# Performance work log

Measured on AMD Instinct MI355X. Metric: run time of the kernel, lower is better.

## Reference

```python
import jax, jax.numpy as jnp
import numpy as np

D = 1024
K = 64
H = 8           # MHA heads
HD = D // H
TEMP = 0.1
B, S = 8, 4096


def setup_inputs() -> dict:
    key = jax.random.key(0)
    ks = jax.random.split(key, 16)
    s = lambda fan_in: 1.0 / np.sqrt(fan_in)
    inp = {
        "x": jax.random.normal(ks[0], (B, S, D), dtype=jnp.float32),
        "efas_scores": jax.random.uniform(ks[1], (B, S), dtype=jnp.float32),
        # energy_projector: Linear(1 -> K)
        "w_e": jax.random.uniform(ks[2], (K,), minval=-1.0, maxval=1.0, dtype=jnp.float32),
        "b_e": jax.random.uniform(ks[3], (K,), minval=-1.0, maxval=1.0, dtype=jnp.float32),
        # routing_mlp: Linear(D->K), ReLU, Linear(K->K); weights stored [in, out]
        "w1": jax.random.uniform(ks[4], (D, K), minval=-s(D), maxval=s(D), dtype=jnp.float32),
        "b1": jax.random.uniform(ks[5], (K,), minval=-s(D), maxval=s(D), dtype=jnp.float32),
        "w2": jax.random.uniform(ks[6], (K, K), minval=-s(K), maxval=s(K), dtype=jnp.float32),
        "b2": jax.random.uniform(ks[7], (K,), minval=-s(K), maxval=s(K), dtype=jnp.float32),
        # MultiheadAttention packed in-proj [D, 3D] and out-proj [D, D]
        "w_qkv": jax.random.uniform(ks[8], (D, 3 * D), minval=-s(D), maxval=s(D), dtype=jnp.float32),
        "b_qkv": jnp.zeros((3 * D,), dtype=jnp.float32),
        "w_o": jax.random.uniform(ks[9], (D, D), minval=-s(D), maxval=s(D), dtype=jnp.float32),
        "b_o": jnp.zeros((D,), dtype=jnp.float32),
        # output_proj: Linear(D -> D)
        "w_p": jax.random.uniform(ks[10], (D, D), minval=-s(D), maxval=s(D), dtype=jnp.float32),
        "b_p": jax.random.uniform(ks[11], (D,), minval=-s(D), maxval=s(D), dtype=jnp.float32),
    }
    return inp


def _mha(a, w_qkv, b_qkv, w_o, b_o):
    # a: [B, K, D] self-attention, 8 heads (eval mode, no dropout)
    b, k, _ = a.shape
    qkv = a @ w_qkv + b_qkv                         # [B, K, 3D]
    q, kk, v = jnp.split(qkv, 3, axis=-1)
    split = lambda t: t.reshape(b, k, H, HD).transpose(0, 2, 1, 3)  # [B,H,K,HD]
    q, kk, v = split(q), split(kk), split(v)
    scores = jnp.einsum('bhqd,bhkd->bhqk', q, kk) / np.sqrt(HD)
    attn = jax.nn.softmax(scores, axis=-1)
    out = jnp.einsum('bhqk,bhkd->bhqd', attn, v)    # [B,H,K,HD]
    out = out.transpose(0, 2, 1, 3).reshape(b, k, D)
    return out @ w_o + b_o


def reference(x, efas_scores, w_e, b_e, w1, b1, w2, b2, w_qkv, b_qkv, w_o, b_o, w_p, b_p):
    # energy routing: Linear(1 -> K) on efas_scores[..., None]
    energy_routing = efas_scores[..., None] * w_e + b_e            # [B,S,K]
    # content routing: Linear(D->K) -> ReLU -> Linear(K->K)
    content_routing = jax.nn.relu(x @ w1 + b1) @ w2 + b2           # [B,S,K]
    # eval-mode combination as in the original (self.training == False)
    routing_logits = energy_routing * 2.0 + content_routing
    routing_weights = jax.nn.softmax(routing_logits / TEMP, axis=-1)  # [B,S,K]
    # token -> anchor weighted aggregation
    anchor_inputs = jnp.einsum('bsk,bsd->bkd', routing_weights, x)    # [B,K,D]
    anchor_outputs = _mha(anchor_inputs, w_qkv, b_qkv, w_o, b_o)      # [B,K,D]
    # anchor -> token scatter-back
    token_outputs = jnp.einsum('bsk,bkd->bsd', routing_weights, anchor_outputs)
    return token_outputs @ w_p + b_p
```

## Files before the change

### kernel.cpp

```cpp
#include <hip/hip_runtime.h>
#include <cstddef>

#define TB 256

constexpr int Bb = 8, Ss = 4096, Dd = 1024, Kk = 64, Hh = 8;
constexpr float INV_TEMP = 10.0f;
constexpr float ATTN_SCALE = 0.08838834764831845f;

constexpr size_t N_RW  = (size_t)Bb * Ss * Kk;
constexpr size_t N_AKD = (size_t)Bb * Kk * Dd;
constexpr size_t OFF_RW  = 0;
constexpr size_t OFF_AI  = OFF_RW  + N_RW;
constexpr size_t OFF_QKV = OFF_AI  + N_AKD;
constexpr size_t OFF_ATT = OFF_QKV + 3 * N_AKD;
constexpr size_t OFF_AO  = OFF_ATT + N_AKD;
constexpr size_t OFF_AOP = OFF_AO  + N_AKD;

typedef __attribute__((ext_vector_type(8))) short bf16x8;
typedef __attribute__((ext_vector_type(4))) float f32x4;

#define MFMA(a, b, c) __builtin_amdgcn_mfma_f32_16x16x32_bf16(a, b, c, 0, 0, 0)

__device__ inline ushort f2bf(float f) {
    union { float f; uint u; } v; v.f = f;
    return (ushort)((v.u + 0x7fffu + ((v.u >> 16) & 1u)) >> 16);
}
__device__ inline float bf2f(ushort h) {
    union { uint u; float f; } v; v.u = ((uint)h) << 16;
    return v.f;
}
__device__ inline void split2(float f, ushort& h, ushort& l) {
    h = f2bf(f);
    l = f2bf(f - bf2f(h));
}

__device__ inline void st4(ushort* t, int row, int s0, ushort4 v) {
    char* p = (char*)t + row * 144 + ((((s0 >> 3) ^ ((row >> 2) & 7)) << 4) | ((s0 & 7) << 1));
    *(ushort4*)p = v;
}
__device__ inline void st1(ushort* t, int row, int s, ushort v) {
    char* p = (char*)t + row * 144 + ((((s >> 3) ^ ((row >> 2) & 7)) << 4) | ((s & 7) << 1));
    *(ushort*)p = v;
}
__device__ inline bf16x8 ldfrag(const ushort* t, int row, int sblk) {
    const char* p = (const char*)t + row * 144 + (((sblk ^ ((row >> 2) & 7))) << 4);
    return *(const bf16x8*)p;
}
__device__ inline void natf(ushort* thi, ushort* tlo, int row, int s0, float4 v) {
    ushort h0,h1,h2,h3,l0,l1,l2,l3;
    split2(v.x,h0,l0); split2(v.y,h1,l1); split2(v.z,h2,l2); split2(v.w,h3,l3);
    st4(thi, row, s0, make_ushort4(h0,h1,h2,h3));
    st4(tlo, row, s0, make_ushort4(l0,l1,l2,l3));
}
__device__ inline void trf(ushort* thi, ushort* tlo, int rowbase, int s0,
                           float4 a, float4 b, float4 c, float4 d) {
    float m[4][4] = {{a.x,b.x,c.x,d.x},{a.y,b.y,c.y,d.y},
                     {a.z,b.z,c.z,d.z},{a.w,b.w,c.w,d.w}};
#pragma unroll
    for (int i = 0; i < 4; ++i) {
        ushort h[4], l[4];
#pragma unroll
        for (int j = 0; j < 4; ++j) split2(m[i][j], h[j], l[j]);
        st4(thi, rowbase + i, s0, make_ushort4(h[0],h[1],h[2],h[3]));
        st4(tlo, rowbase + i, s0, make_ushort4(l[0],l[1],l[2],l[3]));
    }
}
__device__ inline f32x4 mm3(bf16x8 ah, bf16x8 al, bf16x8 bh, bf16x8 bl, f32x4 c) {
    c = MFMA(ah, bh, c);
    c = MFMA(ah, bl, c);
    c = MFMA(al, bh, c);
    return c;
}

__global__ __launch_bounds__(TB) void k_zero(float* __restrict__ p, int n4) {
    int i = blockIdx.x * TB + threadIdx.x;
    if (i < n4) ((float4*)p)[i] = make_float4(0.f, 0.f, 0.f, 0.f);
}

__global__ __launch_bounds__(TB) void k_routing(
    const float* __restrict__ x, const float* __restrict__ efas,
    const float* __restrict__ w_e, const float* __restrict__ b_e,
    const float* __restrict__ w1, const float* __restrict__ b1,
    const float* __restrict__ w2, const float* __restrict__ b2,
    float* __restrict__ rw)
{
    __shared__ __align__(16) ushort xa_hi[128*72], xa_lo[128*72];
    __shared__ __align__(16) ushort wa_hi[64*72],  wa_lo[64*72];
    const int tid = threadIdx.x, lane = tid & 63, wv = tid >> 6;
    const int b = blockIdx.x & 7, t0 = (blockIdx.x >> 3) * 128;
    const int r15 = lane & 15, g = lane >> 4;

    f32x4 acc[2][4];
#pragma unroll
    for (int mt = 0; mt < 2; ++mt)
#pragma unroll
      for (int nt = 0; nt < 4; ++nt) acc[mt][nt] = (f32x4)0.f;

    for (int kc = 0; kc < 16; ++kc) {
        const int k0 = kc * 64;
#pragma unroll
        for (int p = 0; p < 8; ++p) {
            int q = tid + p * TB;
            int row = q >> 4, s0 = (q & 15) << 2;
            float4 v = *(const float4*)&x[((size_t)b*Ss + t0 + row)*Dd + k0 + s0];
            natf(xa_hi, xa_lo, row, s0, v);
        }
        {
            int n0 = (tid & 15) << 2, s0 = (tid >> 4) << 2;
            const float* base = &w1[(size_t)(k0 + s0) * Kk + n0];
            float4 a  = *(const float4*)(base);
            float4 bq = *(const float4*)(base + Kk);
            float4 cq = *(const float4*)(base + 2*Kk);
            float4 dq = *(const float4*)(base + 3*Kk);
            trf(wa_hi, wa_lo, n0, s0, a, bq, cq, dq);
        }
        __syncthreads();
#pragma unroll
        for (int ks = 0; ks < 2; ++ks) {
            bf16x8 ah[2], al[2];
#pragma unroll
            for (int mt = 0; mt < 2; ++mt) {
                int row = wv*32 + mt*16 + r15;
                ah[mt] = ldfrag(xa_hi, row, ks*4 + g);
                al[mt] = ldfrag(xa_lo, row, ks*4 + g);
            }
#pragma unroll
            for (int nt = 0; nt < 4; ++nt) {
                bf16x8 bh = ldfrag(wa_hi, nt*16 + r15, ks*4 + g);
                bf16x8 bl = ldfrag(wa_lo, nt*16 + r15, ks*4 + g);
#pragma unroll
                for (int mt = 0; mt < 2; ++mt)
                    acc[mt][nt] = mm3(ah[mt], al[mt], bh, bl, acc[mt][nt]);
            }
        }
        __syncthreads();
    }
    float b1v[4];
#pragma unroll
    for (int nt = 0; nt < 4; ++nt) b1v[nt] = b1[nt*16 + r15];
#pragma unroll
    for (int mt = 0; mt < 2; ++mt)
#pragma unroll
      for (int nt = 0; nt < 4; ++nt)
#pragma unroll
        for (int j = 0; j < 4; ++j) {
            float hv = fmaxf(acc[mt][nt][j] + b1v[nt], 0.f);
            ushort hh, hl; split2(hv, hh, hl);
            int row = wv*32 + mt*16 + g*4 + j, col = nt*16 + r15;
            st1(xa_hi, row, col, hh);
            st1(xa_lo, row, col, hl);
        }
    {
        int n0 = (tid & 15) << 2, s0 = (tid >> 4) << 2;
        const float* base = &w2[(size_t)s0 * Kk + n0];
        float4 a  = *(const float4*)(base);
        float4 bq = *(const float4*)(base + Kk);
        float4 cq = *(const float4*)(base + 2*Kk);
        float4 dq = *(const float4*)(base + 3*Kk);
        trf(wa_hi, wa_lo, n0, s0, a, bq, cq, dq);
    }
    __syncthreads();

    f32x4 acc2[2][4];
#pragma unroll
    for (int mt = 0; mt < 2; ++mt)
#pragma unroll
      for (int nt = 0; nt < 4; ++nt) acc2[mt][nt] = (f32x4)0.f;
#pragma unroll
    for (int ks = 0; ks < 2; ++ks) {
        bf16x8 ah[2], al[2];
#pragma unroll
        for (int mt = 0; mt < 2; ++mt) {
            int row = wv*32 + mt*16 + r15;
            ah[mt] = ldfrag(xa_hi, row, ks*4 + g);
            al[mt] = ldfrag(xa_lo, row, ks*4 + g);
        }
#pragma unroll
        for (int nt = 0; nt < 4; ++nt) {
            bf16x8 bh = ldfrag(wa_hi, nt*16 + r15, ks*4 + g);
            bf16x8 bl = ldfrag(wa_lo, nt*16 + r15, ks*4 + g);
#pragma unroll
            for (int mt = 0; mt < 2; ++mt)
                acc2[mt][nt] = mm3(ah[mt], al[mt], bh, bl, acc2[mt][nt]);
        }
    }
    float wev[4], bev[4], b2v[4];
#pragma unroll
    for (int nt = 0; nt < 4; ++nt) {
        wev[nt] = w_e[nt*16 + r15]; bev[nt] = b_e[nt*16 + r15]; b2v[nt] = b2[nt*16 + r15];
    }
#pragma unroll
    for (int mt = 0; mt < 2; ++mt)
#pragma unroll
      for (int j = 0; j < 4; ++j) {
        int row = wv*32 + mt*16 + g*4 + j;
        float ef = efas[(size_t)b*Ss + t0 + row];
        float t[4];
#pragma unroll
        for (int nt = 0; nt < 4; ++nt)
            t[nt] = (acc2[mt][nt][j] + b2v[nt] + 2.f*(ef*wev[nt] + bev[nt])) * INV_TEMP;
        float m = fmaxf(fmaxf(t[0],t[1]), fmaxf(t[2],t[3]));
#pragma unroll
        for (int off = 1; off <= 8; off <<= 1) m = fmaxf(m, __shfl_xor(m, off));
        float s = 0.f;
#pragma unroll
        for (int nt = 0; nt < 4; ++nt) { t[nt] = __expf(t[nt] - m); s += t[nt]; }
#pragma unroll
        for (int off = 1; off <= 8; off <<= 1) s += __shfl_xor(s, off);
        float inv = 1.f / s;
#pragma unroll
        for (int nt = 0; nt < 4; ++nt)
            rw[((size_t)b*Ss + t0 + row)*Kk + nt*16 + r15] = t[nt] * inv;
      }
}

__global__ __launch_bounds__(TB) void k_anchor(
    const float* __restrict__ x, const float* __restrict__ rw, float* __restrict__ ai)
{
    __shared__ __align__(16) ushort at_hi[64*72],  at_lo[64*72];
    __shared__ __align__(16) ushort bt_hi[128*72], bt_lo[128*72];
    const int tid = threadIdx.x, lane = tid & 63, wv = tid >> 6;
    const int b = blockIdx.x & 7, dt = (blockIdx.x >> 3) & 7, sc = blockIdx.x >> 6;
    const int r15 = lane & 15, g = lane >> 4;

    f32x4 acc[4][2];
#pragma unroll
    for (int mt = 0; mt < 4; ++mt)
#pragma unroll
      for (int nt = 0; nt < 2; ++nt) acc[mt][nt] = (f32x4)0.f;

    for (int cc = 0; cc < 8; ++cc) {
        const int sb = sc*512 + cc*64;
        {
            int k0 = (tid & 15) << 2, s0 = (tid >> 4) << 2;
            const float* base = &rw[((size_t)b*Ss + sb + s0)*Kk + k0];
            float4 a  = *(const float4*)(base);
            float4 bq = *(const float4*)(base + Kk);
            float4 cq = *(const float4*)(base + 2*Kk);
            float4 dq = *(const float4*)(base + 3*Kk);
            trf(at_hi, at_lo, k0, s0, a, bq, cq, dq);
        }
#pragma unroll
        for (int p = 0; p < 2; ++p) {
            int q = tid + p * TB;
            int d0 = (q & 31) << 2, s0 = (q >> 5) << 2;
            const float* base = &x[((size_t)b*Ss + sb + s0)*Dd + dt*128 + d0];
            float4 a  = *(const float4*)(base);
            float4 bq = *(const float4*)(base + Dd);
            float4 cq = *(const float4*)(base + 2*Dd);
            float4 dq = *(const float4*)(base + 3*Dd);
            trf(bt_hi, bt_lo, d0, s0, a, bq, cq, dq);
        }
        __syncthreads();
#pragma unroll
        for (int ks = 0; ks < 2; ++ks) {
            bf16x8 ah[4], al[4];
#pragma unroll
            for (int mt = 0; mt < 4; ++mt) {
                ah[mt] = ldfrag(at_hi, mt*16 + r15, ks*4 + g);
                al[mt] = ldfrag(at_lo, mt*16 + r15, ks*4 + g);
            }
#pragma unroll
            for (int nt = 0; nt < 2; ++nt) {
                int rn = wv*32 + nt*16 + r15;
                bf16x8 bh = ldfrag(bt_hi, rn, ks*4 + g);
                bf16x8 bl = ldfrag(bt_lo, rn, ks*4 + g);
#pragma unroll
                for (int mt = 0; mt < 4; ++mt)
                    acc[mt][nt] = mm3(ah[mt], al[mt], bh, bl, acc[mt][nt]);
            }
        }
        __syncthreads();
    }
#pragma unroll
    for (int mt = 0; mt < 4; ++mt)
#pragma unroll
      for (int nt = 0; nt < 2; ++nt)
#pragma unroll
        for (int j = 0; j < 4; ++j) {
            int k = mt*16 + g*4 + j;
            int d = dt*128 + wv*32 + nt*16 + r15;
            atomicAdd(&ai[((size_t)b*Kk + k)*Dd + d], acc[mt][nt][j]);
        }
}

template <int KDIM, int NDIM, bool HASBIAS>
__global__ __launch_bounds__(TB) void k_gemm_a(
    const float* __restrict__ A, const float* __restrict__ W,
    const float* __restrict__ bias, float* __restrict__ C)
{
    __shared__ __align__(16) ushort at_hi[64*72],  at_lo[64*72];
    __shared__ __align__(16) ushort bt_hi[128*72], bt_lo[128*72];
    const int tid = threadIdx.x, lane = tid & 63, wv = tid >> 6;
    const int b = blockIdx.x & 7, n0 = (blockIdx.x >> 3) * 128;
    const int r15 = lane & 15, g = lane >> 4;

    f32x4 acc[4][2];
#pragma unroll
    for (int mt = 0; mt < 4; ++mt)
#pragma unroll
      for (int nt = 0; nt < 2; ++nt) acc[mt][nt] = (f32x4)0.f;

    for (int kc = 0; kc < KDIM/64; ++kc) {
        const int k0 = kc * 64;
#pragma unroll
        for (int p = 0; p < 4; ++p) {
            int q = tid + p * TB;
            int row = q >> 4, s0 = (q & 15) << 2;
            float4 v = *(const float4*)&A[((size_t)b*64 + row)*KDIM + k0 + s0];
            natf(at_hi, at_lo, row, s0, v);
        }
#pragma unroll
        for (int p = 0; p < 2; ++p) {
            int q = tid + p * TB;
            int nn0 = (q & 31) << 2, s0 = (q >> 5) << 2;
            const float* base = &W[(size_t)(k0 + s0)*NDIM + n0 + nn0];
            float4 a  = *(const float4*)(base);
            float4 bq = *(const float4*)(base + NDIM);
            float4 cq = *(const float4*)(base + 2*(size_t)NDIM);
            float4 dq = *(const float4*)(base + 3*(size_t)NDIM);
            trf(bt_hi, bt_lo, nn0, s0, a, bq, cq, dq);
        }
        __syncthreads();
#pragma unroll
        for (int ks = 0; ks < 2; ++ks) {
            bf16x8 ah[4], al[4];
#pragma unroll
            for (int mt = 0; mt < 4; ++mt) {
                ah[mt] = ldfrag(at_hi, mt*16 + r15, ks*4 + g);
                al[mt] = ldfrag(at_lo, mt*16 + r15, ks*4 + g);
            }
#pragma unroll
            for (int nt = 0; nt < 2; ++nt) {
                int rn = wv*32 + nt*16 + r15;
                bf16x8 bh = ldfrag(bt_hi, rn, ks*4 + g);
                bf16x8 bl = ldfrag(bt_lo, rn, ks*4 + g);
#pragma unroll
                for (int mt = 0; mt < 4; ++mt)
                    acc[mt][nt] = mm3(ah[mt], al[mt], bh, bl, acc[mt][nt]);
            }
        }
        __syncthreads();
    }
#pragma unroll
    for (int nt = 0; nt < 2; ++nt) {
        int n = n0 + wv*32 + nt*16 + r15;
        float bb = HASBIAS ? bias[n] : 0.f;
#pragma unroll
        for (int mt = 0; mt < 4; ++mt)
#pragma unroll
          for (int j = 0; j < 4; ++j)
            C[((size_t)b*64 + mt*16 + g*4 + j)*NDIM + n] = acc[mt][nt][j] + bb;
    }
}

__global__ __launch_bounds__(TB) void k_attn(
    const float* __restrict__ qkv, float* __restrict__ att)
{
    __shared__ __align__(16) ushort qt_hi[64*72],  qt_lo[64*72];
    __shared__ __align__(16) ushort kt_hi[64*72],  kt_lo[64*72];
    __shared__ __align__(16) ushort vt_hi[128*72], vt_lo[128*72];
    const int tid = threadIdx.x, lane = tid & 63, wv = tid >> 6;
    const int b = blockIdx.x >> 3, h = blockIdx.x & 7;
    const int r15 = lane & 15, g = lane >> 4;

    f32x4 accs[4];
#pragma unroll
    for (int nt = 0; nt < 4; ++nt) accs[nt] = (f32x4)0.f;

    for (int ch = 0; ch < 2; ++ch) {
        const int c0 = h*128 + ch*64;
#pragma unroll
        for (int p = 0; p < 4; ++p) {
            int q = tid + p * TB;
            int row = q >> 4, s0 = (q & 15) << 2;
            size_t base = ((size_t)b*64 + row)*3072 + c0 + s0;
            natf(qt_hi, qt_lo, row, s0, *(const float4*)&qkv[base]);
            natf(kt_hi, kt_lo, row, s0, *(const float4*)&qkv[base + 1024]);
        }
        __syncthreads();
#pragma unroll
        for (int ks = 0; ks < 2; ++ks) {
            bf16x8 ah = ldfrag(qt_hi, wv*16 + r15, ks*4 + g);
            bf16x8 al = ldfrag(qt_lo, wv*16 + r15, ks*4 + g);
#pragma unroll
            for (int nt = 0; nt < 4; ++nt) {
                bf16x8 bh = ldfrag(kt_hi, nt*16 + r15, ks*4 + g);
                bf16x8 bl = ldfrag(kt_lo, nt*16 + r15, ks*4 + g);
                accs[nt] = mm3(ah, al, bh, bl, accs[nt]);
            }
        }
        __syncthreads();
    }
    float pr[4][4];
#pragma unroll
    for (int j = 0; j < 4; ++j) {
        float t[4];
#pragma unroll
        for (int nt = 0; nt < 4; ++nt) t[nt] = accs[nt][j] * ATTN_SCALE;
        float m = fmaxf(fmaxf(t[0],t[1]), fmaxf(t[2],t[3]));
#pragma unroll
        for (int off = 1; off <= 8; off <<= 1) m = fmaxf(m, __shfl_xor(m, off));
        float s = 0.f;
#pragma unroll
        for (int nt = 0; nt < 4; ++nt) { t[nt] = __expf(t[nt] - m); s += t[nt]; }
#pragma unroll
        for (int off = 1; off <= 8; off <<= 1) s += __shfl_xor(s, off);
        float inv = 1.f / s;
#pragma unroll
        for (int nt = 0; nt < 4; ++nt) pr[j][nt] = t[nt] * inv;
    }
#pragma unroll
    for (int j = 0; j < 4; ++j)
#pragma unroll
      for (int nt = 0; nt < 4; ++nt) {
        ushort hh, hl; split2(pr[j][nt], hh, hl);
        st1(qt_hi, wv*16 + g*4 + j, nt*16 + r15, hh);
        st1(qt_lo, wv*16 + g*4 + j, nt*16 + r15, hl);
      }
#pragma unroll
    for (int p = 0; p < 2; ++p) {
        int q = tid + p * TB;
        int d0 = (q & 31) << 2, a0 = (q >> 5) << 2;
        const float* base = &qkv[((size_t)b*64 + a0)*3072 + 2048 + h*128 + d0];
        float4 a  = *(const float4*)(base);
        float4 bq = *(const float4*)(base + 3072);
        float4 cq = *(const float4*)(base + 2*3072);
        float4 dq = *(const float4*)(base + 3*3072);
        trf(vt_hi, vt_lo, d0, a0, a, bq, cq, dq);
    }
    __syncthreads();
    f32x4 acc2[8];
#pragma unroll
    for (int nt = 0; nt < 8; ++nt) acc2[nt] = (f32x4)0.f;
#pragma unroll
    for (int ks = 0; ks < 2; ++ks) {
        bf16x8 ah = ldfrag(qt_hi, wv*16 + r15, ks*4 + g);
        bf16x8 al = ldfrag(qt_lo, wv*16 + r15, ks*4 + g);
#pragma unroll
        for (int nt = 0; nt < 8; ++nt) {
            bf16x8 bh = ldfrag(vt_hi, nt*16 + r15, ks*4 + g);
            bf16x8 bl = ldfrag(vt_lo, nt*16 + r15, ks*4 + g);
            acc2[nt] = mm3(ah, al, bh, bl, acc2[nt]);
        }
    }
#pragma unroll
    for (int nt = 0; nt < 8; ++nt)
#pragma unroll
      for (int j = 0; j < 4; ++j)
        att[((size_t)b*64 + wv*16 + g*4 + j)*1024 + h*128 + nt*16 + r15] = acc2[nt][j];
}

__global__ __launch_bounds__(TB) void k_scatter(
    const float* __restrict__ rw, const float* __restrict__ aop,
    const float* __restrict__ b_p, float* __restrict__ out)
{
    __shared__ __align__(16) ushort at_hi[128*72], at_lo[128*72];
    __shared__ __align__(16) ushort bt_hi[128*72], bt_lo[128*72];
    const int tid = threadIdx.x, lane = tid & 63, wv = tid >> 6;
    const int b = blockIdx.x & 7, st = (blockIdx.x >> 3) & 31, dt = blockIdx.x >> 8;
    const int r15 = lane & 15, g = lane >> 4;
    const int t0 = st * 128;

#pragma unroll
    for (int p = 0; p < 8; ++p) {
        int q = tid + p * TB;
        int row = q >> 4, s0 = (q & 15) << 2;
        float4 v = *(const float4*)&rw[((size_t)b*Ss + t0 + row)*Kk + s0];
        natf(at_hi, at_lo, row, s0, v);
    }
#pragma unroll
    for (int p = 0; p < 2; ++p) {
        int q = tid + p * TB;
        int d0 = (q & 31) << 2, k0q = (q >> 5) << 2;
        const float* base = &aop[((size_t)b*Kk + k0q)*Dd + dt*128 + d0];
        float4 a  = *(const float4*)(base);
        float4 bq = *(const float4*)(base + Dd);
        float4 cq = *(const float4*)(base + 2*Dd);
        float4 dq = *(const float4*)(base + 3*Dd);
        trf(bt_hi, bt_lo, d0, k0q, a, bq, cq, dq);
    }
    __syncthreads();

    f32x4 acc[2][8];
#pragma unroll
    for (int mt = 0; mt < 2; ++mt)
#pragma unroll
      for (int nt = 0; nt < 8; ++nt) acc[mt][nt] = (f32x4)0.f;
#pragma unroll
    for (int ks = 0; ks < 2; ++ks) {
        bf16x8 ah[2], al[2];
#pragma unroll
        for (int mt = 0; mt < 2; ++mt) {
            ah[mt] = ldfrag(at_hi, wv*32 + mt*16 + r15, ks*4 + g);
            al[mt] = ldfrag(at_lo, wv*32 + mt*16 + r15, ks*4 + g);
        }
#pragma unroll
        for (int nt = 0; nt < 8; ++nt) {
            bf16x8 bh = ldfrag(bt_hi, nt*16 + r15, ks*4 + g);
            bf16x8 bl = ldfrag(bt_lo, nt*16 + r15, ks*4 + g);
#pragma unroll
            for (int mt = 0; mt < 2; ++mt)
                acc[mt][nt] = mm3(ah[mt], al[mt], bh, bl, acc[mt][nt]);
        }
    }
#pragma unroll
    for (int nt = 0; nt < 8; ++nt) {
        float bb = b_p[dt*128 + nt*16 + r15];
#pragma unroll
        for (int mt = 0; mt < 2; ++mt)
#pragma unroll
          for (int j = 0; j < 4; ++j)
            out[((size_t)b*Ss + t0 + wv*32 + mt*16 + g*4 + j)*Dd + dt*128 + nt*16 + r15]
                = acc[mt][nt][j] + bb;
    }
}

extern "C" void kernel_launch(void* const* d_in, const int* in_sizes, int n_in,
                              void* d_out, int out_size, void* d_ws, size_t ws_size,
                              hipStream_t stream)
{
    const float* x     = (const float*)d_in[0];
    const float* efas  = (const float*)d_in[1];
    const float* w_e   = (const float*)d_in[2];
    const float* b_e   = (const float*)d_in[3];
    const float* w1    = (const float*)d_in[4];
    const float* b1    = (const float*)d_in[5];
    const float* w2    = (const float*)d_in[6];
    const float* b2    = (const float*)d_in[7];
    const float* w_qkv = (const float*)d_in[8];
    const float* b_qkv = (const float*)d_in[9];
    const float* w_o   = (const float*)d_in[10];
    const float* b_o   = (const float*)d_in[11];
    const float* w_p   = (const float*)d_in[12];
    const float* b_p   = (const float*)d_in[13];
    float* out = (float*)d_out;
    float* ws  = (float*)d_ws;

    float* rw  = ws + OFF_RW;
    float* ai  = ws + OFF_AI;
    float* qkv = ws + OFF_QKV;
    float* att = ws + OFF_ATT;
    float* ao  = ws + OFF_AO;
    float* aop = ws + OFF_AOP;

    hipLaunchKernelGGL(k_zero, dim3(512), dim3(TB), 0, stream, ai, (int)(N_AKD/4));
    hipLaunchKernelGGL(k_routing, dim3(256), dim3(TB), 0, stream,
                       x, efas, w_e, b_e, w1, b1, w2, b2, rw);
    hipLaunchKernelGGL(k_anchor, dim3(512), dim3(TB), 0, stream, x, rw, ai);
    hipLaunchKernelGGL((k_gemm_a<1024, 3072, true>), dim3(192), dim3(TB), 0, stream,
                       ai, w_qkv, b_qkv, qkv);
    hipLaunchKernelGGL(k_attn, dim3(64), dim3(TB), 0, stream, qkv, att);
    hipLaunchKernelGGL((k_gemm_a<1024, 1024, true>), dim3(64), dim3(TB), 0, stream,
                       att, w_o, b_o, ao);
    hipLaunchKernelGGL((k_gemm_a<1024, 1024, false>), dim3(64), dim3(TB), 0, stream,
                       ao, w_p, nullptr, aop);
    hipLaunchKernelGGL(k_scatter, dim3(2048), dim3(TB), 0, stream, rw, aop, b_p, out);
}
```

Baseline: 262.9 us.

## Pre-split weights to bf16 hi/lo, split-K routing with atomics, drop LDS staging

Adds a prep kernel that transposes all weights once per call and splits them into bf16 hi/lo arrays, so the GEMM kernels load MFMA fragments directly from global memory without LDS staging or per-block conversion. Routing is split into a split-K first layer (atomics into a zeroed buffer) and a second kernel that writes routing weights as pre-split bf16. The anchor and scatter kernels use new tilings and read the pre-split data; the output-projection GEMM writes a transposed pre-split result for the scatter. This trades extra kernel launches, atomic traffic and a per-call weight conversion for less redundant conversion and fewer LDS round trips.

Result: slower. 355.9 us (+35.4%).

```diff
diff --git a/kernel.cpp b/kernel.cpp
--- a/kernel.cpp
+++ b/kernel.cpp
@@ -7,19 +7,38 @@
 constexpr float INV_TEMP = 10.0f;
 constexpr float ATTN_SCALE = 0.08838834764831845f;
 
-constexpr size_t N_RW  = (size_t)Bb * Ss * Kk;
-constexpr size_t N_AKD = (size_t)Bb * Kk * Dd;
-constexpr size_t OFF_RW  = 0;
-constexpr size_t OFF_AI  = OFF_RW  + N_RW;
-constexpr size_t OFF_QKV = OFF_AI  + N_AKD;
-constexpr size_t OFF_ATT = OFF_QKV + 3 * N_AKD;
-constexpr size_t OFF_AO  = OFF_ATT + N_AKD;
-constexpr size_t OFF_AOP = OFF_AO  + N_AKD;
-
 typedef __attribute__((ext_vector_type(8))) short bf16x8;
 typedef __attribute__((ext_vector_type(4))) float f32x4;
 
 #define MFMA(a, b, c) __builtin_amdgcn_mfma_f32_16x16x32_bf16(a, b, c, 0, 0, 0)
+
+constexpr size_t OFF_G   = 0;
+constexpr size_t SZ_G    = (size_t)Bb*Ss*Kk*4;
+constexpr size_t OFF_AI  = OFF_G + SZ_G;
+constexpr size_t SZ_AKD  = (size_t)Bb*Kk*Dd*4;
+constexpr size_t OFF_QKV = OFF_AI + SZ_AKD;
+constexpr size_t OFF_ATT = OFF_QKV + 3*SZ_AKD;
+constexpr size_t OFF_AO  = OFF_ATT + SZ_AKD;
+constexpr size_t OFF_RWH = OFF_AO + SZ_AKD;
+constexpr size_t SZ_RW2  = (size_t)Bb*Ss*Kk*2;
+constexpr size_t OFF_RWL = OFF_RWH + SZ_RW2;
+constexpr size_t OFF_APH = OFF_RWL + SZ_RW2;
+constexpr size_t SZ_AP2  = (size_t)Bb*Dd*Kk*2;
+constexpr size_t OFF_APL = OFF_APH + SZ_AP2;
+constexpr size_t OFF_W1H = OFF_APL + SZ_AP2;
+constexpr size_t SZ_W1   = (size_t)Kk*Dd*2;
+constexpr size_t OFF_W1L = OFF_W1H + SZ_W1;
+constexpr size_t OFF_W2H = OFF_W1L + SZ_W1;
+constexpr size_t SZ_W2   = (size_t)Kk*Kk*2;
+constexpr size_t OFF_W2L = OFF_W2H + SZ_W2;
+constexpr size_t OFF_WQH = OFF_W2L + SZ_W2;
+constexpr size_t SZ_WQ   = (size_t)3*Dd*Dd*2;
+constexpr size_t OFF_WQL = OFF_WQH + SZ_WQ;
+constexpr size_t OFF_WOH = OFF_WQL + SZ_WQ;
+constexpr size_t SZ_WD   = (size_t)Dd*Dd*2;
+constexpr size_t OFF_WOL = OFF_WOH + SZ_WD;
+constexpr size_t OFF_WPH = OFF_WOL + SZ_WD;
+constexpr size_t OFF_WPL = OFF_WPH + SZ_WD;
 
 __device__ inline ushort f2bf(float f) {
     union { float f; uint u; } v; v.f = f;
@@ -32,6 +51,20 @@
 __device__ inline void split2(float f, ushort& h, ushort& l) {
     h = f2bf(f);
     l = f2bf(f - bf2f(h));
+}
+__device__ inline void cvt8(float4 a, float4 b, bf16x8& h8, bf16x8& l8) {
+    float f[8] = {a.x, a.y, a.z, a.w, b.x, b.y, b.z, b.w};
+#pragma unroll
+    for (int i = 0; i < 8; ++i) {
+        ushort hh, ll; split2(f[i], hh, ll);
+        h8[i] = (short)hh; l8[i] = (short)ll;
+    }
+}
+__device__ inline f32x4 mm3(bf16x8 ah, bf16x8 al, bf16x8 bh, bf16x8 bl, f32x4 c) {
+    c = MFMA(ah, bh, c);
+    c = MFMA(ah, bl, c);
+    c = MFMA(al, bh, c);
+    return c;
 }
 
 __device__ inline void st4(ushort* t, int row, int s0, ushort4 v) {
@@ -65,11 +98,12 @@
         st4(tlo, rowbase + i, s0, make_ushort4(l[0],l[1],l[2],l[3]));
     }
 }
-__device__ inline f32x4 mm3(bf16x8 ah, bf16x8 al, bf16x8 bh, bf16x8 bl, f32x4 c) {
-    c = MFMA(ah, bh, c);
-    c = MFMA(ah, bl, c);
-    c = MFMA(al, bh, c);
-    return c;
+__device__ inline void trfb(ushort* t, int rowbase, int s0,
+                            ushort4 r0, ushort4 r1, ushort4 r2, ushort4 r3) {
+    st4(t, rowbase + 0, s0, make_ushort4(r0.x, r1.x, r2.x, r3.x));
+    st4(t, rowbase + 1, s0, make_ushort4(r0.y, r1.y, r2.y, r3.y));
+    st4(t, rowbase + 2, s0, make_ushort4(r0.z, r1.z, r2.z, r3.z));
+    st4(t, rowbase + 3, s0, make_ushort4(r0.w, r1.w, r2.w, r3.w));
 }
 
 __global__ __launch_bounds__(TB) void k_zero(float* __restrict__ p, int n4) {
@@ -77,129 +111,139 @@
     if (i < n4) ((float4*)p)[i] = make_float4(0.f, 0.f, 0.f, 0.f);
 }
 
-__global__ __launch_bounds__(TB) void k_routing(
-    const float* __restrict__ x, const float* __restrict__ efas,
+__global__ __launch_bounds__(TB) void k_prep(
+    const float* __restrict__ w1, const float* __restrict__ w2,
+    const float* __restrict__ wq, const float* __restrict__ wo,
+    const float* __restrict__ wp,
+    ushort* __restrict__ w1h, ushort* __restrict__ w1l,
+    ushort* __restrict__ w2h, ushort* __restrict__ w2l,
+    ushort* __restrict__ wqh, ushort* __restrict__ wql,
+    ushort* __restrict__ woh, ushort* __restrict__ wol,
+    ushort* __restrict__ wph, ushort* __restrict__ wpl)
+{
+    __shared__ float t[64][64];
+    const int blk = blockIdx.x, tid = threadIdx.x;
+    const float* in; ushort* oh; ushort* ol; int R, IC, r0, c0;
+    if (blk < 16)        { in = w1; oh = w1h; ol = w1l; R = 1024; IC = 64;
+                           r0 = blk * 64; c0 = 0; }
+    else if (blk == 16)  { in = w2; oh = w2h; ol = w2l; R = 64;   IC = 64;
+                           r0 = 0; c0 = 0; }
+    else if (blk < 785)  { int i = blk - 17; in = wq; oh = wqh; ol = wql;
+                           R = 1024; IC = 3072; r0 = (i / 48) * 64; c0 = (i % 48) * 64; }
+    else if (blk < 1041) { int i = blk - 785; in = wo; oh = woh; ol = wol;
+                           R = 1024; IC = 1024; r0 = (i / 16) * 64; c0 = (i % 16) * 64; }
+    else                 { int i = blk - 1041; in = wp; oh = wph; ol = wpl;
+                           R = 1024; IC = 1024; r0 = (i / 16) * 64; c0 = (i % 16) * 64; }
+
+    {
+        int r = tid >> 2, cq = (tid & 3) * 16;
+        const float* ip = &in[(size_t)(r0 + r) * IC + c0 + cq];
+#pragma unroll
+        for (int q = 0; q < 4; ++q)
+            *(float4*)&t[r][cq + q * 4] = *(const float4*)(ip + q * 4);
+    }
+    __syncthreads();
+    {
+        int oc = tid & 63, or0 = (tid >> 6) * 16;
+        ushort th[16], tl[16];
+#pragma unroll
+        for (int i = 0; i < 16; ++i) split2(t[or0 + i][oc], th[i], tl[i]);
+        size_t base = (size_t)(c0 + oc) * R + r0 + or0;
+#pragma unroll
+        for (int q = 0; q < 4; ++q) {
+            *(ushort4*)&oh[base + q * 4] = make_ushort4(th[q*4], th[q*4+1], th[q*4+2], th[q*4+3]);
+            *(ushort4*)&ol[base + q * 4] = make_ushort4(tl[q*4], tl[q*4+1], tl[q*4+2], tl[q*4+3]);
+        }
+    }
+}
+
+__global__ __launch_bounds__(TB) void k_route1(
+    const float* __restrict__ x, const ushort* __restrict__ w1h,
+    const ushort* __restrict__ w1l, float* __restrict__ g)
+{
+    const int tid = threadIdx.x, lane = tid & 63, wv = tid >> 6;
+    const int r15 = lane & 15, gg = lane >> 4;
+    const int b = blockIdx.x & 7, st = (blockIdx.x >> 3) & 63, dh = blockIdx.x >> 9;
+    const int t0 = st * 64;
+
+    const float* xrow = &x[((size_t)b*Ss + t0 + wv*16 + r15)*Dd + dh*512 + gg*8];
+
+    f32x4 acc[4];
+#pragma unroll
+    for (int nt = 0; nt < 4; ++nt) acc[nt] = (f32x4)0.f;
+
+    for (int kc = 0; kc < 16; ++kc) {
+        float4 xa = *(const float4*)(xrow + kc * 32);
+        float4 xb = *(const float4*)(xrow + kc * 32 + 4);
+        bf16x8 ah, al; cvt8(xa, xb, ah, al);
+#pragma unroll
+        for (int nt = 0; nt < 4; ++nt) {
+            size_t wi = (size_t)(nt*16 + r15)*Dd + dh*512 + kc*32 + gg*8;
+            bf16x8 bh = *(const bf16x8*)&w1h[wi];
+            bf16x8 bl = *(const bf16x8*)&w1l[wi];
+            acc[nt] = mm3(ah, al, bh, bl, acc[nt]);
+        }
+    }
+#pragma unroll
+    for (int nt = 0; nt < 4; ++nt)
+#pragma unroll
+      for (int j = 0; j < 4; ++j) {
+        int row = t0 + wv*16 + gg*4 + j;
+        atomicAdd(&g[((size_t)b*Ss + row)*Kk + nt*16 + r15], acc[nt][j]);
+      }
+}
+
+__global__ __launch_bounds__(TB) void k_route2(
+    const float* __restrict__ g, const float* __restrict__ efas,
     const float* __restrict__ w_e, const float* __restrict__ b_e,
-    const float* __restrict__ w1, const float* __restrict__ b1,
-    const float* __restrict__ w2, const float* __restrict__ b2,
-    float* __restrict__ rw)
-{
-    __shared__ __align__(16) ushort xa_hi[128*72], xa_lo[128*72];
-    __shared__ __align__(16) ushort wa_hi[64*72],  wa_lo[64*72];
+    const float* __restrict__ b1, const ushort* __restrict__ w2h,
+    const ushort* __restrict__ w2l, const float* __restrict__ b2,
+    ushort* __restrict__ rwh, ushort* __restrict__ rwl)
+{
     const int tid = threadIdx.x, lane = tid & 63, wv = tid >> 6;
-    const int b = blockIdx.x & 7, t0 = (blockIdx.x >> 3) * 128;
-    const int r15 = lane & 15, g = lane >> 4;
-
-    f32x4 acc[2][4];
-#pragma unroll
-    for (int mt = 0; mt < 2; ++mt)
-#pragma unroll
-      for (int nt = 0; nt < 4; ++nt) acc[mt][nt] = (f32x4)0.f;
-
-    for (int kc = 0; kc < 16; ++kc) {
-        const int k0 = kc * 64;
-#pragma unroll
-        for (int p = 0; p < 8; ++p) {
-            int q = tid + p * TB;
-            int row = q >> 4, s0 = (q & 15) << 2;
-            float4 v = *(const float4*)&x[((size_t)b*Ss + t0 + row)*Dd + k0 + s0];
-            natf(xa_hi, xa_lo, row, s0, v);
-        }
-        {
-            int n0 = (tid & 15) << 2, s0 = (tid >> 4) << 2;
-            const float* base = &w1[(size_t)(k0 + s0) * Kk + n0];
-            float4 a  = *(const float4*)(base);
-            float4 bq = *(const float4*)(base + Kk);
-            float4 cq = *(const float4*)(base + 2*Kk);
-            float4 dq = *(const float4*)(base + 3*Kk);
-            trf(wa_hi, wa_lo, n0, s0, a, bq, cq, dq);
-        }
-        __syncthreads();
-#pragma unroll
-        for (int ks = 0; ks < 2; ++ks) {
-            bf16x8 ah[2], al[2];
-#pragma unroll
-            for (int mt = 0; mt < 2; ++mt) {
-                int row = wv*32 + mt*16 + r15;
-                ah[mt] = ldfrag(xa_hi, row, ks*4 + g);
-                al[mt] = ldfrag(xa_lo, row, ks*4 + g);
-            }
-#pragma unroll
-            for (int nt = 0; nt < 4; ++nt) {
-                bf16x8 bh = ldfrag(wa_hi, nt*16 + r15, ks*4 + g);
-                bf16x8 bl = ldfrag(wa_lo, nt*16 + r15, ks*4 + g);
-#pragma unroll
-                for (int mt = 0; mt < 2; ++mt)
-                    acc[mt][nt] = mm3(ah[mt], al[mt], bh, bl, acc[mt][nt]);
-            }
-        }
-        __syncthreads();
-    }
-    float b1v[4];
-#pragma unroll
-    for (int nt = 0; nt < 4; ++nt) b1v[nt] = b1[nt*16 + r15];
-#pragma unroll
-    for (int mt = 0; mt < 2; ++mt)
-#pragma unroll
-      for (int nt = 0; nt < 4; ++nt)
-#pragma unroll
-        for (int j = 0; j < 4; ++j) {
-            float hv = fmaxf(acc[mt][nt][j] + b1v[nt], 0.f);
-            ushort hh, hl; split2(hv, hh, hl);
-            int row = wv*32 + mt*16 + g*4 + j, col = nt*16 + r15;
-            st1(xa_hi, row, col, hh);
-            st1(xa_lo, row, col, hl);
-        }
-    {
-        int n0 = (tid & 15) << 2, s0 = (tid >> 4) << 2;
-        const float* base = &w2[(size_t)s0 * Kk + n0];
-        float4 a  = *(const float4*)(base);
-        float4 bq = *(const float4*)(base + Kk);
-        float4 cq = *(const float4*)(base + 2*Kk);
-        float4 dq = *(const float4*)(base + 3*Kk);
-        trf(wa_hi, wa_lo, n0, s0, a, bq, cq, dq);
-    }
-    __syncthreads();
-
-    f32x4 acc2[2][4];
-#pragma unroll
-    for (int mt = 0; mt < 2; ++mt)
-#pragma unroll
-      for (int nt = 0; nt < 4; ++nt) acc2[mt][nt] = (f32x4)0.f;
+    const int r15 = lane & 15, gg = lane >> 4;
+    const int b = blockIdx.x & 7, t0 = (blockIdx.x >> 3) * 64;
+
+    bf16x8 ah[2], al[2];
 #pragma unroll
     for (int ks = 0; ks < 2; ++ks) {
-        bf16x8 ah[2], al[2];
-#pragma unroll
-        for (int mt = 0; mt < 2; ++mt) {
-            int row = wv*32 + mt*16 + r15;
-            ah[mt] = ldfrag(xa_hi, row, ks*4 + g);
-            al[mt] = ldfrag(xa_lo, row, ks*4 + g);
-        }
-#pragma unroll
-        for (int nt = 0; nt < 4; ++nt) {
-            bf16x8 bh = ldfrag(wa_hi, nt*16 + r15, ks*4 + g);
-            bf16x8 bl = ldfrag(wa_lo, nt*16 + r15, ks*4 + g);
-#pragma unroll
-            for (int mt = 0; mt < 2; ++mt)
-                acc2[mt][nt] = mm3(ah[mt], al[mt], bh, bl, acc2[mt][nt]);
-        }
-    }
+        const float* gp = &g[((size_t)b*Ss + t0 + wv*16 + r15)*Kk + ks*32 + gg*8];
+        float4 a = *(const float4*)gp, bq = *(const float4*)(gp + 4);
+        float4 ba = *(const float4*)&b1[ks*32 + gg*8];
+        float4 bb = *(const float4*)&b1[ks*32 + gg*8 + 4];
+        a.x = fmaxf(a.x + ba.x, 0.f); a.y = fmaxf(a.y + ba.y, 0.f);
+        a.z = fmaxf(a.z + ba.z, 0.f); a.w = fmaxf(a.w + ba.w, 0.f);
+        bq.x = fmaxf(bq.x + bb.x, 0.f); bq.y = fmaxf(bq.y + bb.y, 0.f);
+        bq.z = fmaxf(bq.z + bb.z, 0.f); bq.w = fmaxf(bq.w + bb.w, 0.f);
+        cvt8(a, bq, ah[ks], al[ks]);
+    }
+    f32x4 acc[4];
+#pragma unroll
+    for (int nt = 0; nt < 4; ++nt) acc[nt] = (f32x4)0.f;
+#pragma unroll
+    for (int ks = 0; ks < 2; ++ks)
+#pragma unroll
+      for (int nt = 0; nt < 4; ++nt) {
+        size_t wi = (size_t)(nt*16 + r15)*Kk + ks*32 + gg*8;
+        bf16x8 bh = *(const bf16x8*)&w2h[wi];
+        bf16x8 bl = *(const bf16x8*)&w2l[wi];
+        acc[nt] = mm3(ah[ks], al[ks], bh, bl, acc[nt]);
+      }
+
     float wev[4], bev[4], b2v[4];
 #pragma unroll
     for (int nt = 0; nt < 4; ++nt) {
         wev[nt] = w_e[nt*16 + r15]; bev[nt] = b_e[nt*16 + r15]; b2v[nt] = b2[nt*16 + r15];
     }
 #pragma unroll
-    for (int mt = 0; mt < 2; ++mt)
-#pragma unroll
-      for (int j = 0; j < 4; ++j) {
-        int row = wv*32 + mt*16 + g*4 + j;
-        float ef = efas[(size_t)b*Ss + t0 + row];
+    for (int j = 0; j < 4; ++j) {
+        int row = t0 + wv*16 + gg*4 + j;
+        float ef = efas[(size_t)b*Ss + row];
         float t[4];
 #pragma unroll
         for (int nt = 0; nt < 4; ++nt)
-            t[nt] = (acc2[mt][nt][j] + b2v[nt] + 2.f*(ef*wev[nt] + bev[nt])) * INV_TEMP;
-        float m = fmaxf(fmaxf(t[0],t[1]), fmaxf(t[2],t[3]));
+            t[nt] = (acc[nt][j] + b2v[nt] + 2.f*(ef*wev[nt] + bev[nt])) * INV_TEMP;
+        float m = fmaxf(fmaxf(t[0], t[1]), fmaxf(t[2], t[3]));
 #pragma unroll
         for (int off = 1; off <= 8; off <<= 1) m = fmaxf(m, __shfl_xor(m, off));
         float s = 0.f;
@@ -209,148 +253,119 @@
         for (int off = 1; off <= 8; off <<= 1) s += __shfl_xor(s, off);
         float inv = 1.f / s;
 #pragma unroll
-        for (int nt = 0; nt < 4; ++nt)
-            rw[((size_t)b*Ss + t0 + row)*Kk + nt*16 + r15] = t[nt] * inv;
-      }
+        for (int nt = 0; nt < 4; ++nt) {
+            ushort hh, hl; split2(t[nt] * inv, hh, hl);
+            size_t o = ((size_t)b*Ss + row)*Kk + nt*16 + r15;
+            rwh[o] = hh; rwl[o] = hl;
+        }
+    }
 }
 
 __global__ __launch_bounds__(TB) void k_anchor(
-    const float* __restrict__ x, const float* __restrict__ rw, float* __restrict__ ai)
-{
-    __shared__ __align__(16) ushort at_hi[64*72],  at_lo[64*72];
-    __shared__ __align__(16) ushort bt_hi[128*72], bt_lo[128*72];
+    const float* __restrict__ x, const ushort* __restrict__ rwh,
+    const ushort* __restrict__ rwl, float* __restrict__ ai)
+{
+    __shared__ __align__(16) ushort rt_h[64*72], rt_l[64*72];
+    __shared__ __align__(16) ushort xt_h[64*72], xt_l[64*72];
     const int tid = threadIdx.x, lane = tid & 63, wv = tid >> 6;
-    const int b = blockIdx.x & 7, dt = (blockIdx.x >> 3) & 7, sc = blockIdx.x >> 6;
-    const int r15 = lane & 15, g = lane >> 4;
+    const int r15 = lane & 15, gg = lane >> 4;
+    const int b = blockIdx.x & 7, dt = (blockIdx.x >> 3) & 15, sc = blockIdx.x >> 7;
+
+    f32x4 acc[4];
+#pragma unroll
+    for (int mt = 0; mt < 4; ++mt) acc[mt] = (f32x4)0.f;
+
+    const int k0 = (tid & 15) * 4, s0q = (tid >> 4) * 4;
+    for (int ss = 0; ss < 8; ++ss) {
+        const int sb = sc*512 + ss*64;
+        {
+            const ushort* rp = &rwh[((size_t)b*Ss + sb + s0q)*Kk + k0];
+            trfb(rt_h, k0, s0q, *(const ushort4*)rp, *(const ushort4*)(rp + Kk),
+                 *(const ushort4*)(rp + 2*Kk), *(const ushort4*)(rp + 3*Kk));
+            const ushort* rp2 = &rwl[((size_t)b*Ss + sb + s0q)*Kk + k0];
+            trfb(rt_l, k0, s0q, *(const ushort4*)rp2, *(const ushort4*)(rp2 + Kk),
+                 *(const ushort4*)(rp2 + 2*Kk), *(const ushort4*)(rp2 + 3*Kk));
+        }
+        {
+            const float* xp = &x[((size_t)b*Ss + sb + s0q)*Dd + dt*64 + k0];
+            trf(xt_h, xt_l, k0, s0q, *(const float4*)xp, *(const float4*)(xp + Dd),
+                *(const float4*)(xp + 2*Dd), *(const float4*)(xp + 3*Dd));
+        }
+        __syncthreads();
+#pragma unroll
+        for (int ks = 0; ks < 2; ++ks) {
+            bf16x8 bh = ldfrag(xt_h, wv*16 + r15, ks*4 + gg);
+            bf16x8 bl = ldfrag(xt_l, wv*16 + r15, ks*4 + gg);
+#pragma unroll
+            for (int mt = 0; mt < 4; ++mt) {
+                bf16x8 ah = ldfrag(rt_h, mt*16 + r15, ks*4 + gg);
+                bf16x8 al = ldfrag(rt_l, mt*16 + r15, ks*4 + gg);
+                acc[mt] = mm3(ah, al, bh, bl, acc[mt]);
+            }
+        }
+        __syncthreads();
+    }
+#pragma unroll
+    for (int mt = 0; mt < 4; ++mt)
+#pragma unroll
+      for (int j = 0; j < 4; ++j)
+        atomicAdd(&ai[((size_t)b*Kk + mt*16 + gg*4 + j)*Dd + dt*64 + wv*16 + r15],
+                  acc[mt][j]);
+}
+
+template <int NDIM, bool HASBIAS, bool TRANSOUT>
+__global__ __launch_bounds__(TB) void k_gemm(
+    const float* __restrict__ A, const ushort* __restrict__ WH,
+    const ushort* __restrict__ WL, const float* __restrict__ bias,
+    float* __restrict__ C, ushort* __restrict__ TH, ushort* __restrict__ TL)
+{
+    const int tid = threadIdx.x, lane = tid & 63, wv = tid >> 6;
+    const int r15 = lane & 15, gg = lane >> 4;
+    constexpr int NT = NDIM / 128;
+    const int b = blockIdx.x / NT, n0 = (blockIdx.x % NT) * 128;
 
     f32x4 acc[4][2];
 #pragma unroll
     for (int mt = 0; mt < 4; ++mt)
 #pragma unroll
-      for (int nt = 0; nt < 2; ++nt) acc[mt][nt] = (f32x4)0.f;
-
-    for (int cc = 0; cc < 8; ++cc) {
-        const int sb = sc*512 + cc*64;
-        {
-            int k0 = (tid & 15) << 2, s0 = (tid >> 4) << 2;
-            const float* base = &rw[((size_t)b*Ss + sb + s0)*Kk + k0];
-            float4 a  = *(const float4*)(base);
-            float4 bq = *(const float4*)(base + Kk);
-            float4 cq = *(const float4*)(base + 2*Kk);
-            float4 dq = *(const float4*)(base + 3*Kk);
-            trf(at_hi, at_lo, k0, s0, a, bq, cq, dq);
-        }
-#pragma unroll
-        for (int p = 0; p < 2; ++p) {
-            int q = tid + p * TB;
-            int d0 = (q & 31) << 2, s0 = (q >> 5) << 2;
-            const float* base = &x[((size_t)b*Ss + sb + s0)*Dd + dt*128 + d0];
-            float4 a  = *(const float4*)(base);
-            float4 bq = *(const float4*)(base + Dd);
-            float4 cq = *(const float4*)(base + 2*Dd);
-            float4 dq = *(const float4*)(base + 3*Dd);
-            trf(bt_hi, bt_lo, d0, s0, a, bq, cq, dq);
-        }
-        __syncthreads();
-#pragma unroll
-        for (int ks = 0; ks < 2; ++ks) {
-            bf16x8 ah[4], al[4];
-#pragma unroll
-            for (int mt = 0; mt < 4; ++mt) {
-                ah[mt] = ldfrag(at_hi, mt*16 + r15, ks*4 + g);
-                al[mt] = ldfrag(at_lo, mt*16 + r15, ks*4 + g);
+      for (int nl = 0; nl < 2; ++nl) acc[mt][nl] = (f32x4)0.f;
+
+    for (int kc = 0; kc < 32; ++kc) {
+        const int kb = kc * 32;
+        bf16x8 ah[4], al[4];
+#pragma unroll
+        for (int mt = 0; mt < 4; ++mt) {
+            const float* ap = &A[((size_t)b*64 + mt*16 + r15)*Dd + kb + gg*8];
+            cvt8(*(const float4*)ap, *(const float4*)(ap + 4), ah[mt], al[mt]);
+        }
+#pragma unroll
+        for (int nl = 0; nl < 2; ++nl) {
+            size_t wi = (size_t)(n0 + wv*32 + nl*16 + r15)*Dd + kb + gg*8;
+            bf16x8 bh = *(const bf16x8*)&WH[wi];
+            bf16x8 bl = *(const bf16x8*)&WL[wi];
+#pragma unroll
+            for (int mt = 0; mt < 4; ++mt)
+                acc[mt][nl] = mm3(ah[mt], al[mt], bh, bl, acc[mt][nl]);
+        }
+    }
+#pragma unroll
+    for (int nl = 0; nl < 2; ++nl) {
+        int col = n0 + wv*32 + nl*16 + r15;
+        float bb = HASBIAS ? bias[col] : 0.f;
+#pragma unroll
+        for (int mt = 0; mt < 4; ++mt)
+#pragma unroll
+          for (int j = 0; j < 4; ++j) {
+            int mrow = mt*16 + gg*4 + j;
+            float v = acc[mt][nl][j] + bb;
+            if (TRANSOUT) {
+                ushort hh, hl; split2(v, hh, hl);
+                size_t o = ((size_t)b*Dd + col)*Kk + mrow;
+                TH[o] = hh; TL[o] = hl;
+            } else {
+                C[((size_t)b*64 + mrow)*NDIM + col] = v;
             }
-#pragma unroll
-            for (int nt = 0; nt < 2; ++nt) {
-                int rn = wv*32 + nt*16 + r15;
-                bf16x8 bh = ldfrag(bt_hi, rn, ks*4 + g);
-                bf16x8 bl = ldfrag(bt_lo, rn, ks*4 + g);
-#pragma unroll
-                for (int mt = 0; mt < 4; ++mt)
-                    acc[mt][nt] = mm3(ah[mt], al[mt], bh, bl, acc[mt][nt]);
-            }
-        }
-        __syncthreads();
-    }
-#pragma unroll
-    for (int mt = 0; mt < 4; ++mt)
-#pragma unroll
-      for (int nt = 0; nt < 2; ++nt)
-#pragma unroll
-        for (int j = 0; j < 4; ++j) {
-            int k = mt*16 + g*4 + j;
-            int d = dt*128 + wv*32 + nt*16 + r15;
-            atomicAdd(&ai[((size_t)b*Kk + k)*Dd + d], acc[mt][nt][j]);
-        }
-}
-
-template <int KDIM, int NDIM, bool HASBIAS>
-__global__ __launch_bounds__(TB) void k_gemm_a(
-    const float* __restrict__ A, const float* __restrict__ W,
-    const float* __restrict__ bias, float* __restrict__ C)
-{
-    __shared__ __align__(16) ushort at_hi[64*72],  at_lo[64*72];
-    __shared__ __align__(16) ushort bt_hi[128*72], bt_lo[128*72];
-    const int tid = threadIdx.x, lane = tid & 63, wv = tid >> 6;
-    const int b = blockIdx.x & 7, n0 = (blockIdx.x >> 3) * 128;
-    const int r15 = lane & 15, g = lane >> 4;
-
-    f32x4 acc[4][2];
-#pragma unroll
-    for (int mt = 0; mt < 4; ++mt)
-#pragma unroll
-      for (int nt = 0; nt < 2; ++nt) acc[mt][nt] = (f32x4)0.f;
-
-    for (int kc = 0; kc < KDIM/64; ++kc) {
-        const int k0 = kc * 64;
-#pragma unroll
-        for (int p = 0; p < 4; ++p) {
-            int q = tid + p * TB;
-            int row = q >> 4, s0 = (q & 15) << 2;
-            float4 v = *(const float4*)&A[((size_t)b*64 + row)*KDIM + k0 + s0];
-            natf(at_hi, at_lo, row, s0, v);
-        }
-#pragma unroll
-        for (int p = 0; p < 2; ++p) {
-            int q = tid + p * TB;
-            int nn0 = (q & 31) << 2, s0 = (q >> 5) << 2;
-            const float* base = &W[(size_t)(k0 + s0)*NDIM + n0 + nn0];
-            float4 a  = *(const float4*)(base);
-            float4 bq = *(const float4*)(base + NDIM);
-            float4 cq = *(const float4*)(base + 2*(size_t)NDIM);
-            float4 dq = *(const float4*)(base + 3*(size_t)NDIM);
-            trf(bt_hi, bt_lo, nn0, s0, a, bq, cq, dq);
-        }
-        __syncthreads();
-#pragma unroll
-        for (int ks = 0; ks < 2; ++ks) {
-            bf16x8 ah[4], al[4];
-#pragma unroll
-            for (int mt = 0; mt < 4; ++mt) {
-                ah[mt] = ldfrag(at_hi, mt*16 + r15, ks*4 + g);
-                al[mt] = ldfrag(at_lo, mt*16 + r15, ks*4 + g);
-            }
-#pragma unroll
-            for (int nt = 0; nt < 2; ++nt) {
-                int rn = wv*32 + nt*16 + r15;
-                bf16x8 bh = ldfrag(bt_hi, rn, ks*4 + g);
-                bf16x8 bl = ldfrag(bt_lo, rn, ks*4 + g);
-#pragma unroll
-                for (int mt = 0; mt < 4; ++mt)
-                    acc[mt][nt] = mm3(ah[mt], al[mt], bh, bl, acc[mt][nt]);
-            }
-        }
-        __syncthreads();
-    }
-#pragma unroll
-    for (int nt = 0; nt < 2; ++nt) {
-        int n = n0 + wv*32 + nt*16 + r15;
-        float bb = HASBIAS ? bias[n] : 0.f;
-#pragma unroll
-        for (int mt = 0; mt < 4; ++mt)
-#pragma unroll
-          for (int j = 0; j < 4; ++j)
-            C[((size_t)b*64 + mt*16 + g*4 + j)*NDIM + n] = acc[mt][nt][j] + bb;
+          }
     }
 }
 
@@ -452,53 +467,35 @@
 }
 
 __global__ __launch_bounds__(TB) void k_scatter(
-    const float* __restrict__ rw, const float* __restrict__ aop,
+    const ushort* __restrict__ rwh, const ushort* __restrict__ rwl,
+    const ushort* __restrict__ aph, const ushort* __restrict__ apl,
     const float* __restrict__ b_p, float* __restrict__ out)
 {
-    __shared__ __align__(16) ushort at_hi[128*72], at_lo[128*72];
-    __shared__ __align__(16) ushort bt_hi[128*72], bt_lo[128*72];
     const int tid = threadIdx.x, lane = tid & 63, wv = tid >> 6;
+    const int r15 = lane & 15, gg = lane >> 4;
     const int b = blockIdx.x & 7, st = (blockIdx.x >> 3) & 31, dt = blockIdx.x >> 8;
-    const int r15 = lane & 15, g = lane >> 4;
     const int t0 = st * 128;
 
-#pragma unroll
-    for (int p = 0; p < 8; ++p) {
-        int q = tid + p * TB;
-        int row = q >> 4, s0 = (q & 15) << 2;
-        float4 v = *(const float4*)&rw[((size_t)b*Ss + t0 + row)*Kk + s0];
-        natf(at_hi, at_lo, row, s0, v);
-    }
-#pragma unroll
-    for (int p = 0; p < 2; ++p) {
-        int q = tid + p * TB;
-        int d0 = (q & 31) << 2, k0q = (q >> 5) << 2;
-        const float* base = &aop[((size_t)b*Kk + k0q)*Dd + dt*128 + d0];
-        float4 a  = *(const float4*)(base);
-        float4 bq = *(const float4*)(base + Dd);
-        float4 cq = *(const float4*)(base + 2*Dd);
-        float4 dq = *(const float4*)(base + 3*Dd);
-        trf(bt_hi, bt_lo, d0, k0q, a, bq, cq, dq);
-    }
-    __syncthreads();
-
     f32x4 acc[2][8];
 #pragma unroll
     for (int mt = 0; mt < 2; ++mt)
 #pragma unroll
       for (int nt = 0; nt < 8; ++nt) acc[mt][nt] = (f32x4)0.f;
+
 #pragma unroll
     for (int ks = 0; ks < 2; ++ks) {
         bf16x8 ah[2], al[2];
 #pragma unroll
         for (int mt = 0; mt < 2; ++mt) {
-            ah[mt] = ldfrag(at_hi, wv*32 + mt*16 + r15, ks*4 + g);
-            al[mt] = ldfrag(at_lo, wv*32 + mt*16 + r15, ks*4 + g);
+            size_t ri = ((size_t)b*Ss + t0 + wv*32 + mt*16 + r15)*Kk + ks*32 + gg*8;
+            ah[mt] = *(const bf16x8*)&rwh[ri];
+            al[mt] = *(const bf16x8*)&rwl[ri];
         }
 #pragma unroll
         for (int nt = 0; nt < 8; ++nt) {
-            bf16x8 bh = ldfrag(bt_hi, nt*16 + r15, ks*4 + g);
-            bf16x8 bl = ldfrag(bt_lo, nt*16 + r15, ks*4 + g);
+            size_t bi = ((size_t)b*Dd + dt*128 + nt*16 + r15)*Kk + ks*32 + gg*8;
+            bf16x8 bh = *(const bf16x8*)&aph[bi];
+            bf16x8 bl = *(const bf16x8*)&apl[bi];
 #pragma unroll
             for (int mt = 0; mt < 2; ++mt)
                 acc[mt][nt] = mm3(ah[mt], al[mt], bh, bl, acc[mt][nt]);
@@ -506,13 +503,13 @@
     }
 #pragma unroll
     for (int nt = 0; nt < 8; ++nt) {
-        float bb = b_p[dt*128 + nt*16 + r15];
+        float bp = b_p[dt*128 + nt*16 + r15];
 #pragma unroll
         for (int mt = 0; mt < 2; ++mt)
 #pragma unroll
           for (int j = 0; j < 4; ++j)
-            out[((size_t)b*Ss + t0 + wv*32 + mt*16 + g*4 + j)*Dd + dt*128 + nt*16 + r15]
-                = acc[mt][nt][j] + bb;
+            out[((size_t)b*Ss + t0 + wv*32 + mt*16 + gg*4 + j)*Dd + dt*128 + nt*16 + r15]
+                = acc[mt][nt][j] + bp;
     }
 }
 
@@ -535,25 +532,44 @@
     const float* w_p   = (const float*)d_in[12];
     const float* b_p   = (const float*)d_in[13];
     float* out = (float*)d_out;
-    float* ws  = (float*)d_ws;
-
-    float* rw  = ws + OFF_RW;
-    float* ai  = ws + OFF_AI;
-    float* qkv = ws + OFF_QKV;
-    float* att = ws + OFF_ATT;
-    float* ao  = ws + OFF_AO;
-    float* aop = ws + OFF_AOP;
-
-    hipLaunchKernelGGL(k_zero, dim3(512), dim3(TB), 0, stream, ai, (int)(N_AKD/4));
-    hipLaunchKernelGGL(k_routing, dim3(256), dim3(TB), 0, stream,
-                       x, efas, w_e, b_e, w1, b1, w2, b2, rw);
-    hipLaunchKernelGGL(k_anchor, dim3(512), dim3(TB), 0, stream, x, rw, ai);
-    hipLaunchKernelGGL((k_gemm_a<1024, 3072, true>), dim3(192), dim3(TB), 0, stream,
-                       ai, w_qkv, b_qkv, qkv);
+    char* ws = (char*)d_ws;
+
+    float*  g   = (float*)(ws + OFF_G);
+    float*  ai  = (float*)(ws + OFF_AI);
+    float*  qkv = (float*)(ws + OFF_QKV);
+    float*  att = (float*)(ws + OFF_ATT);
+    float*  ao  = (float*)(ws + OFF_AO);
+    ushort* rwh = (ushort*)(ws + OFF_RWH);
+    ushort* rwl = (ushort*)(ws + OFF_RWL);
+    ushort* aph = (ushort*)(ws + OFF_APH);
+    ushort* apl = (ushort*)(ws + OFF_APL);
+    ushort* w1h = (ushort*)(ws + OFF_W1H);
+    ushort* w1l = (ushort*)(ws + OFF_W1L);
+    ushort* w2h = (ushort*)(ws + OFF_W2H);
+    ushort* w2l = (ushort*)(ws + OFF_W2L);
+    ushort* wqh = (ushort*)(ws + OFF_WQH);
+    ushort* wql = (ushort*)(ws + OFF_WQL);
+    ushort* woh = (ushort*)(ws + OFF_WOH);
+    ushort* wol = (ushort*)(ws + OFF_WOL);
+    ushort* wph = (ushort*)(ws + OFF_WPH);
+    ushort* wpl = (ushort*)(ws + OFF_WPL);
+
+    hipLaunchKernelGGL(k_prep, dim3(1297), dim3(TB), 0, stream,
+                       w1, w2, w_qkv, w_o, w_p,
+                       w1h, w1l, w2h, w2l, wqh, wql, woh, wol, wph, wpl);
+    hipLaunchKernelGGL(k_zero, dim3(2560), dim3(TB), 0, stream,
+                       g, (int)((SZ_G + SZ_AKD) / 16));
+    hipLaunchKernelGGL(k_route1, dim3(1024), dim3(TB), 0, stream, x, w1h, w1l, g);
+    hipLaunchKernelGGL(k_route2, dim3(512), dim3(TB), 0, stream,
+                       g, efas, w_e, b_e, b1, w2h, w2l, b2, rwh, rwl);
+    hipLaunchKernelGGL(k_anchor, dim3(1024), dim3(TB), 0, stream, x, rwh, rwl, ai);
+    hipLaunchKernelGGL((k_gemm<3072, true, false>), dim3(192), dim3(TB), 0, stream,
+                       ai, wqh, wql, b_qkv, qkv, (ushort*)nullptr, (ushort*)nullptr);
     hipLaunchKernelGGL(k_attn, dim3(64), dim3(TB), 0, stream, qkv, att);
-    hipLaunchKernelGGL((k_gemm_a<1024, 1024, true>), dim3(64), dim3(TB), 0, stream,
-                       att, w_o, b_o, ao);
-    hipLaunchKernelGGL((k_gemm_a<1024, 1024, false>), dim3(64), dim3(TB), 0, stream,
-                       ao, w_p, nullptr, aop);
-    hipLaunchKernelGGL(k_scatter, dim3(2048), dim3(TB), 0, stream, rw, aop, b_p, out);
-}
+    hipLaunchKernelGGL((k_gemm<1024, true, false>), dim3(64), dim3(TB), 0, stream,
+                       att, woh, wol, b_o, ao, (ushort*)nullptr, (ushort*)nullptr);
+    hipLaunchKernelGGL((k_gemm<1024, false, true>), dim3(64), dim3(TB), 0, stream,
+                       ao, wph, wpl, (const float*)nullptr, (float*)nullptr, aph, apl);
+    hipLaunchKernelGGL(k_scatter, dim3(2048), dim3(TB), 0, stream,
+                       rwh, rwl, aph, apl, b_p, out);
+}
```
